# Kernel optimization log

Hardware: AMD Instinct MI355X
Metric: run time of the kernel (lower is better)

## Reference

```python
import jax, jax.numpy as jnp
import numpy as np

D_MODEL = 1024
N_HEADS = 16
D_K = D_MODEL // N_HEADS
D_FF = 4096
EPS = 1e-5


def _layernorm(x, g, b):
    mu = jnp.mean(x, axis=-1, keepdims=True)
    var = jnp.var(x, axis=-1, keepdims=True)
    return (x - mu) * jax.lax.rsqrt(var + EPS) * g + b


def setup_inputs() -> dict:
    key = jax.random.key(0)
    ks = jax.random.split(key, 12)
    s = 0.02
    x = jax.random.normal(ks[0], (2, 2048, D_MODEL), dtype=jnp.float32)
    # Linear weights stored [in, out] so y = x @ W + b
    wq = jax.random.normal(ks[1], (D_MODEL, D_MODEL), dtype=jnp.float32) * s
    wk = jax.random.normal(ks[2], (D_MODEL, D_MODEL), dtype=jnp.float32) * s
    wv = jax.random.normal(ks[3], (D_MODEL, D_MODEL), dtype=jnp.float32) * s
    wo = jax.random.normal(ks[4], (D_MODEL, D_MODEL), dtype=jnp.float32) * s
    bq = jnp.zeros((D_MODEL,), jnp.float32)
    bk = jnp.zeros((D_MODEL,), jnp.float32)
    bv = jnp.zeros((D_MODEL,), jnp.float32)
    bo = jnp.zeros((D_MODEL,), jnp.float32)
    ln1_g = jnp.ones((D_MODEL,), jnp.float32)
    ln1_b = jnp.zeros((D_MODEL,), jnp.float32)
    ln2_g = jnp.ones((D_MODEL,), jnp.float32)
    ln2_b = jnp.zeros((D_MODEL,), jnp.float32)
    w1 = jax.random.normal(ks[5], (D_MODEL, D_FF), dtype=jnp.float32) * s
    b1 = jnp.zeros((D_FF,), jnp.float32)
    w2 = jax.random.normal(ks[6], (D_FF, D_MODEL), dtype=jnp.float32) * s
    b2 = jnp.zeros((D_MODEL,), jnp.float32)
    return {"x": x, "wq": wq, "bq": bq, "wk": wk, "bk": bk, "wv": wv, "bv": bv,
            "wo": wo, "bo": bo, "ln1_g": ln1_g, "ln1_b": ln1_b,
            "ln2_g": ln2_g, "ln2_b": ln2_b, "w1": w1, "b1": b1, "w2": w2, "b2": b2}


def reference(x, wq, bq, wk, bk, wv, bv, wo, bo, ln1_g, ln1_b, ln2_g, ln2_b, w1, b1, w2, b2):
    B, S, _ = x.shape
    res = x
    # project and split heads: [B, S, H, Dk]
    q = (x @ wq + bq).reshape(B, S, N_HEADS, D_K)
    k = (x @ wk + bk).reshape(B, S, N_HEADS, D_K)
    v = (x @ wv + bv).reshape(B, S, N_HEADS, D_K)
    # full score matrix [B, H, Sq, Sk] (faithful to unfused original)
    scores = jnp.einsum('bqhd,bkhd->bhqk', q, k) / jnp.sqrt(jnp.float32(D_K))
    weights = jax.nn.softmax(scores, axis=-1)
    attn = jnp.einsum('bhqk,bkhd->bqhd', weights, v).reshape(B, S, D_MODEL)
    x = _layernorm(res + attn @ wo + bo, ln1_g, ln1_b)
    res = x
    h = jax.nn.relu(x @ w1 + b1)
    x = _layernorm(res + h @ w2 + b2, ln2_g, ln2_b)
    return x
```

## Files before the change

### kernel.cpp

```cpp
#include <hip/hip_runtime.h>
#include <hip/hip_bf16.h>
#include <stdint.h>


typedef __hip_bfloat16 bf16;
typedef short bf16x8 __attribute__((ext_vector_type(8)));
typedef float f32x4 __attribute__((ext_vector_type(4)));

#if __has_builtin(__builtin_amdgcn_exp2f)
#define EXP2F(x) __builtin_amdgcn_exp2f(x)
#else
#define EXP2F(x) exp2f(x)
#endif

__device__ __forceinline__ float bf2f_lo(unsigned u) { return __uint_as_float(u << 16); }
__device__ __forceinline__ float bf2f_hi(unsigned u) { return __uint_as_float(u & 0xffff0000u); }
__device__ __forceinline__ ushort f2bf(float f) {
  union { bf16 h; ushort u; } c; c.h = __float2bfloat16(f); return c.u;
}
__device__ __forceinline__ uint pk_bf16(float a, float b) {
  union { __hip_bfloat162 h2; uint u; } c;
  c.h2 = __float22bfloat162_rn(make_float2(a, b));
  return c.u;
}
__device__ __forceinline__ bool is_f32(const uint* probe) { return probe[0] == 0x3F800000u; }
__device__ __forceinline__ float ld_param(const void* p, size_t i, bool f32) {
  return f32 ? ((const float*)p)[i] : __bfloat162float(((const bf16*)p)[i]);
}

__device__ __forceinline__ void barrier_raw() {
  asm volatile("" ::: "memory");
  __builtin_amdgcn_s_barrier();
  asm volatile("" ::: "memory");
}
__device__ __forceinline__ void lgkm0() {
  asm volatile("s_waitcnt lgkmcnt(0)" ::: "memory");
}
__device__ __forceinline__ void glds16(const ushort* g, ushort* l) {
  __builtin_amdgcn_global_load_lds(
      (const __attribute__((address_space(1))) void*)g,
      (__attribute__((address_space(3))) void*)l, 16, 0, 0);
}

#define MFMA16(MH, NH)                                                        \
  do {                                                                        \
    _Pragma("unroll") for (int c_ = 0; c_ < 2; ++c_)                          \
    _Pragma("unroll") for (int fi_ = 0; fi_ < 4; ++fi_)                       \
    _Pragma("unroll") for (int gi_ = 0; gi_ < 2; ++gi_)                       \
      acc[(MH) * 4 + fi_][(NH) * 2 + gi_] =                                   \
          __builtin_amdgcn_mfma_f32_16x16x32_bf16(                            \
              areg[fi_][c_], breg[(NH) * 2 + gi_][c_],                        \
              acc[(MH) * 4 + fi_][(NH) * 2 + gi_], 0, 0, 0);                  \
  } while (0)

__device__ __forceinline__ void gemm256_body(
    const ushort* __restrict__ A, const ushort* __restrict__ BT,
    const void* __restrict__ bias, const void* __restrict__ res,
    void* __restrict__ C, int N_, int K_, int bm, int bn,
    int kb, int ke, int mode, const uint* probe) {
  __shared__ ushort As[2][16384];
  __shared__ ushort Bs[2][16384];

  const int tid = threadIdx.x;
  const int wave = tid >> 6;
  const int lane = tid & 63;
  const int wm = wave >> 2;
  const int wn = wave & 3;
  const int m16 = lane & 15;
  const int quad = lane >> 4;
  const int nt = (ke - kb) >> 6;

  const int srow = lane >> 2;
  const int skc = ((lane & 3) * 8) ^ (((lane >> 5) & 1) << 4);
  const ushort* pA = A + (size_t)(bm * 256 + wave * 16 + srow) * K_ + kb + skc;
  const ushort* pB = BT + (size_t)(bn * 256 + wave * 16 + srow) * K_ + kb + skc;
  const size_t hstep = (size_t)128 * K_;
  ushort* dA = &As[0][0] + wave * 1024;
  ushort* dB = &Bs[0][0] + wave * 1024;

  auto stageA = [&](int b, int half, int t) {
    const ushort* g = pA + (size_t)half * hstep + t * 64;
    ushort* d = dA + b * 16384 + half * 8192;
    glds16(g, d);
    glds16(g + 32, d + 512);
  };
  auto stageB = [&](int b, int half, int t) {
    const ushort* g = pB + (size_t)half * hstep + t * 64;
    ushort* d = dB + b * 16384 + half * 8192;
    glds16(g, d);
    glds16(g + 32, d + 512);
  };

  const int fr_off = m16 * 32 + ((quad * 8) ^ (((m16 >> 3) & 1) << 4));
  const ushort* rA = &As[0][0] + fr_off;
  const ushort* rB = &Bs[0][0] + fr_off;
  auto ldA = [&](int b, int f, int c) {
    return *(const bf16x8*)(rA + b * 16384 +
                            ((f >> 2) * 8 + wm * 4 + (f & 3)) * 1024 + c * 512);
  };
  auto ldB = [&](int b, int g, int c) {
    return *(const bf16x8*)(rB + b * 16384 +
                            ((g >> 1) * 8 + wn * 2 + (g & 1)) * 1024 + c * 512);
  };

  f32x4 acc[8][4];
#pragma unroll
  for (int f = 0; f < 8; ++f)
#pragma unroll
    for (int g = 0; g < 4; ++g) acc[f][g] = (f32x4){0.f, 0.f, 0.f, 0.f};
  bf16x8 areg[4][2], breg[4][2];

  stageA(0, 0, 0); stageB(0, 0, 0); stageA(0, 1, 0); stageB(0, 1, 0);
  if (nt > 1) { stageA(1, 0, 1); stageB(1, 0, 1); }
  asm volatile("s_waitcnt vmcnt(4)" ::: "memory");
  barrier_raw();

  for (int t = 0; t < nt; ++t) {
    const int b = t & 1, bo = b ^ 1;
#pragma unroll
    for (int fi = 0; fi < 4; ++fi) { areg[fi][0] = ldA(b, fi, 0); areg[fi][1] = ldA(b, fi, 1); }
#pragma unroll
    for (int gi = 0; gi < 2; ++gi) { breg[gi][0] = ldB(b, gi, 0); breg[gi][1] = ldB(b, gi, 1); }
    if (t + 1 < nt) stageA(bo, 1, t + 1);
    barrier_raw(); lgkm0();
    __builtin_amdgcn_s_setprio(1); MFMA16(0, 0); __builtin_amdgcn_s_setprio(0);
    barrier_raw();
#pragma unroll
    for (int gi = 2; gi < 4; ++gi) { breg[gi][0] = ldB(b, gi, 0); breg[gi][1] = ldB(b, gi, 1); }
    if (t + 1 < nt) stageB(bo, 1, t + 1);
    barrier_raw(); lgkm0();
    __builtin_amdgcn_s_setprio(1); MFMA16(0, 1); __builtin_amdgcn_s_setprio(0);
    barrier_raw();
#pragma unroll
    for (int fi = 0; fi < 4; ++fi) { areg[fi][0] = ldA(b, fi + 4, 0); areg[fi][1] = ldA(b, fi + 4, 1); }
    if (t + 2 < nt) stageA(b, 0, t + 2);
    barrier_raw(); lgkm0();
    __builtin_amdgcn_s_setprio(1); MFMA16(1, 0); __builtin_amdgcn_s_setprio(0);
    barrier_raw();
    if (t + 2 < nt) stageB(b, 0, t + 2);
    barrier_raw(); lgkm0();
    __builtin_amdgcn_s_setprio(1); MFMA16(1, 1); __builtin_amdgcn_s_setprio(0);
    if (t + 2 < nt) asm volatile("s_waitcnt vmcnt(4)" ::: "memory");
    else            asm volatile("s_waitcnt vmcnt(0)" ::: "memory");
    barrier_raw();
  }

  const bool F32 = is_f32(probe);
#pragma unroll
  for (int g = 0; g < 4; ++g) {
    const int col = bn * 256 + (g >> 1) * 128 + wn * 32 + (g & 1) * 16 + m16;
    const float bv = (mode >= 3) ? 0.f : ld_param(bias, col, F32);
#pragma unroll
    for (int f = 0; f < 8; ++f) {
      const int rowb = bm * 256 + (f >> 2) * 128 + wm * 64 + (f & 3) * 16 + quad * 4;
#pragma unroll
      for (int r = 0; r < 4; ++r) {
        const int row = rowb + r;
        float v = acc[f][g][r] + bv;
        if (mode == 1) v = fmaxf(v, 0.f);
        if (mode == 2) v += __bfloat162float(((const bf16*)res)[(size_t)row * N_ + col]);
        if (mode == 2 || mode == 3) ((float*)C)[(size_t)row * N_ + col] = v;
        else ((bf16*)C)[(size_t)row * N_ + col] = __float2bfloat16(v);
      }
    }
  }
}

__global__ __launch_bounds__(512, 2) void gemm256_qkv(
    const ushort* A, const ushort* BT0, const ushort* BT1, const ushort* BT2,
    const void* b0, const void* b1, const void* b2,
    bf16* C0, bf16* C1, bf16* C2, const uint* probe) {
  const int sel = blockIdx.y >> 2, bn = blockIdx.y & 3;
  const ushort* BT = sel == 0 ? BT0 : (sel == 1 ? BT1 : BT2);
  const void* bb = sel == 0 ? b0 : (sel == 1 ? b1 : b2);
  bf16* C = sel == 0 ? C0 : (sel == 1 ? C1 : C2);
  gemm256_body(A, BT, bb, nullptr, C, 1024, 1024, blockIdx.x, bn, 0, 1024, 0, probe);
}
__global__ __launch_bounds__(512, 2) void gemm256_ffn1(
    const ushort* A, const ushort* BT, const void* bias, bf16* C, const uint* probe) {
  gemm256_body(A, BT, bias, nullptr, C, 4096, 1024,
               blockIdx.x, blockIdx.y, 0, 1024, 1, probe);
}
__global__ __launch_bounds__(512, 2) void gemm256_ffn2_sk4(
    const ushort* A, const ushort* BT,
    bf16* P0, bf16* P1, bf16* P2, bf16* P3, const uint* probe) {
  const int kz = blockIdx.z;
  bf16* C = kz == 0 ? P0 : kz == 1 ? P1 : kz == 2 ? P2 : P3;
  gemm256_body(A, BT, nullptr, nullptr, C, 1024, 4096, blockIdx.x, blockIdx.y,
               kz * 1024, kz * 1024 + 1024, 4, probe);
}
__global__ __launch_bounds__(512, 2) void gemm256_wo_sk4(
    const ushort* A, const ushort* BT,
    bf16* P0, bf16* P1, bf16* P2, bf16* P3, const uint* probe) {
  const int kz = blockIdx.z;
  bf16* C = kz == 0 ? P0 : kz == 1 ? P1 : kz == 2 ? P2 : P3;
  gemm256_body(A, BT, nullptr, nullptr, C, 1024, 1024, blockIdx.x, blockIdx.y,
               kz * 256, kz * 256 + 256, 4, probe);
}

__global__ __launch_bounds__(256) void transpose_all(
    const void* W0, const void* W1, const void* W2, const void* W3,
    const void* W4, const void* W5, const void* X6,
    ushort* D0, ushort* D1, ushort* D2, ushort* D3, ushort* D4, ushort* D5,
    ushort* D6, const uint* probe) {
  const int z = blockIdx.z;
  if (z == 6) {
    const bool F32 = is_f32(probe);
    const size_t i =
        ((size_t)(blockIdx.y * 128 + blockIdx.x) * 256 + threadIdx.x) * 4;
    if (F32) {
      const float4 a = *(const float4*)((const float*)X6 + i);
      uint2 o; o.x = pk_bf16(a.x, a.y); o.y = pk_bf16(a.z, a.w);
      *(uint2*)(D6 + i) = o;
    } else {
      *(uint2*)(D6 + i) = *(const uint2*)((const ushort*)X6 + i);
    }
    return;
  }
  if (z < 4 && blockIdx.x >= 32) return;
  int n0, k0, K_, N_;
  const void* W;
  ushort* D;
  if (z < 4) {
    n0 = blockIdx.x * 32; k0 = blockIdx.y * 32; K_ = 1024; N_ = 1024;
    W = z == 0 ? W0 : z == 1 ? W1 : z == 2 ? W2 : W3;
    D = z == 0 ? D0 : z == 1 ? D1 : z == 2 ? D2 : D3;
  } else if (z == 4) {
    n0 = blockIdx.x * 32; k0 = blockIdx.y * 32; K_ = 1024; N_ = 4096; W = W4; D = D4;
  } else {
    n0 = blockIdx.y * 32; k0 = blockIdx.x * 32; K_ = 4096; N_ = 1024; W = W5; D = D5;
  }
  const bool F32 = is_f32(probe);
  __shared__ ushort tile[32][33];
  const int tx = threadIdx.x & 31, ty = threadIdx.x >> 5;
#pragma unroll
  for (int i = 0; i < 32; i += 8) {
    const size_t src = (size_t)(k0 + ty + i) * N_ + n0 + tx;
    tile[ty + i][tx] = F32 ? f2bf(((const float*)W)[src]) : ((const ushort*)W)[src];
  }
  __syncthreads();
#pragma unroll
  for (int i = 0; i < 32; i += 8)
    D[(size_t)(n0 + ty + i) * K_ + k0 + tx] = tile[tx][ty + i];
}

__global__ __launch_bounds__(256) void transpose_v(
    const ushort* __restrict__ Vb, ushort* __restrict__ VTp) {
  __shared__ ushort t64[64][66];
  const int tid = threadIdx.x;
  const int ktb = blockIdx.x;
  const int bh = blockIdx.y;
  const int bb = bh >> 4, h = bh & 15;
  const size_t hb = ((size_t)bb * 2048) * 1024 + (size_t)h * 64;
  const int r = tid >> 2, c4 = (tid & 3) * 16;
  const ushort* src = Vb + hb + (size_t)(ktb * 64 + r) * 1024 + c4;
  *(uint4*)&t64[r][c4] = *(const uint4*)src;
  *(uint4*)&t64[r][c4 + 8] = *(const uint4*)(src + 8);
  __syncthreads();
  ushort vals[16];
#pragma unroll
  for (int j = 0; j < 16; ++j) {
    const int jj = c4 + j;
    const int k = 16 * (jj & 3) + 4 * ((jj >> 3) & 3) + 2 * (jj >> 5) + ((jj & 7) >> 2);
    vals[j] = t64[k][r];
  }
  ushort* dst = VTp + (size_t)bh * 131072 + (size_t)r * 2048 + ktb * 64 + c4;
  *(uint4*)dst = *(uint4*)&vals[0];
  *(uint4*)(dst + 8) = *(uint4*)&vals[8];
}

template <bool OUT_EXT, bool RES_EXT>
__global__ __launch_bounds__(256) void ln4_kernel(
    const ushort* __restrict__ P0, const ushort* __restrict__ P1,
    const ushort* __restrict__ P2, const ushort* __restrict__ P3,
    const void* __restrict__ res, const void* __restrict__ bias,
    const void* __restrict__ g, const void* __restrict__ bta,
    void* __restrict__ out, const uint* probe) {
  const bool F32 = is_f32(probe);
  const int row = blockIdx.x;
  const int tid = threadIdx.x;
  const size_t base = (size_t)row * 1024 + tid * 4;
  float xv[4];
  if (RES_EXT && F32) {
    const float4 a = *(const float4*)((const float*)res + base);
    xv[0] = a.x; xv[1] = a.y; xv[2] = a.z; xv[3] = a.w;
  } else {
    const uint2 ur = *(const uint2*)((const ushort*)res + base);
    xv[0] = bf2f_lo(ur.x); xv[1] = bf2f_hi(ur.x);
    xv[2] = bf2f_lo(ur.y); xv[3] = bf2f_hi(ur.y);
  }
#pragma unroll
  for (int i = 0; i < 4; ++i) xv[i] += ld_param(bias, tid * 4 + i, F32);
  auto addv = [&](const ushort* P) {
    const uint2 u = *(const uint2*)(P + base);
    xv[0] += bf2f_lo(u.x); xv[1] += bf2f_hi(u.x);
    xv[2] += bf2f_lo(u.y); xv[3] += bf2f_hi(u.y);
  };
  addv(P0); addv(P1); addv(P2); addv(P3);
  float s = xv[0] + xv[1] + xv[2] + xv[3];
  float ss = xv[0] * xv[0] + xv[1] * xv[1] + xv[2] * xv[2] + xv[3] * xv[3];
#pragma unroll
  for (int o = 32; o > 0; o >>= 1) { s += __shfl_down(s, o); ss += __shfl_down(ss, o); }
  __shared__ float red[8];
  if ((tid & 63) == 0) { red[tid >> 6] = s; red[4 + (tid >> 6)] = ss; }
  __syncthreads();
  s = red[0] + red[1] + red[2] + red[3];
  ss = red[4] + red[5] + red[6] + red[7];
  const float mu = s * (1.f / 1024.f);
  const float rstd = rsqrtf(ss * (1.f / 1024.f) - mu * mu + 1e-5f);
#pragma unroll
  for (int i = 0; i < 4; ++i) {
    const size_t idx = base + i;
    const float y = (xv[i] - mu) * rstd * ld_param(g, tid * 4 + i, F32) +
                    ld_param(bta, tid * 4 + i, F32);
    if (OUT_EXT && F32) ((float*)out)[idx] = y;
    else ((bf16*)out)[idx] = __float2bfloat16(y);
  }
}

__global__ __launch_bounds__(256, 4) void attn_mfma(
    const ushort* __restrict__ Qm, const ushort* __restrict__ Km,
    const ushort* __restrict__ VTp, ushort* __restrict__ Om) {
  __shared__ ushort Ks[2][4096];
  __shared__ ushort Vs[2][4096];

  const int tid = threadIdx.x;
  const int wave = tid >> 6, lane = tid & 63;
  const int m16 = lane & 15, quad = lane >> 4;

  const int g = blockIdx.x;
  const int slot = g >> 3;
  const int bh = (g & 7) * 4 + (slot >> 5);
  const int qt = slot & 31;
  const int bb = bh >> 4, h = bh & 15;
  const size_t hb = ((size_t)bb * 2048) * 1024 + (size_t)h * 64;
  const size_t vo = (size_t)bh * 131072;
  const int q0 = qt * 64 + wave * 16;

  const float QS = 0.125f * 1.44269504f;
  const int swz = (m16 >> 3) << 4;
  const int rdo = m16 * 32 + ((quad * 8) ^ swz);

  bf16x8 qf[2];
#pragma unroll
  for (int c = 0; c < 2; ++c) {
    const uint4 u = *(const uint4*)(Qm + hb + (size_t)(q0 + m16) * 1024 + c * 32 + quad * 8);
    const uint w[4] = {u.x, u.y, u.z, u.w};
    bf16x8 f;
#pragma unroll
    for (int j = 0; j < 4; ++j) {
      const uint p = pk_bf16(bf2f_lo(w[j]) * QS, bf2f_hi(w[j]) * QS);
      f[2 * j]     = (short)(p & 0xffffu);
      f[2 * j + 1] = (short)(p >> 16);
    }
    qf[c] = f;
  }

  f32x4 zero = {0.f, 0.f, 0.f, 0.f};
  f32x4 acc[4];
#pragma unroll
  for (int jd = 0; jd < 4; ++jd) acc[jd] = zero;
  float lp = 0.f;

  const int srow = lane >> 2;
  const int skc = ((lane & 3) * 8) ^ ((lane >> 5) << 4);
  const ushort* pK = Km + hb + (size_t)(wave * 16 + srow) * 1024 + skc;
  const ushort* pV = VTp + vo + (size_t)(wave * 16 + srow) * 2048 + skc;
  ushort* dK = &Ks[0][0] + wave * 1024;
  ushort* dV = &Vs[0][0] + wave * 1024;

  glds16(pK, dK);
  glds16(pK + 32, dK + 512);
  glds16(pV, dV);
  glds16(pV + 32, dV + 512);
  asm volatile("s_waitcnt vmcnt(0)" ::: "memory");

  for (int kt = 0; kt < 2048; kt += 64) {
    const int b = (kt >> 6) & 1;
    __syncthreads();
    if (kt + 64 < 2048) {
      const ushort* gk = pK + (size_t)(kt + 64) * 1024;
      const ushort* gv = pV + (kt + 64);
      ushort* dk2 = dK + (b ^ 1) * 4096;
      ushort* dv2 = dV + (b ^ 1) * 4096;
      glds16(gk, dk2);
      glds16(gk + 32, dk2 + 512);
      glds16(gv, dv2);
      glds16(gv + 32, dv2 + 512);
    }

    f32x4 s[4];
#pragma unroll
    for (int jn = 0; jn < 4; ++jn) s[jn] = zero;
    __builtin_amdgcn_s_setprio(1);
#pragma unroll
    for (int c = 0; c < 2; ++c) {
      bf16x8 kb4[4];
#pragma unroll
      for (int jn = 0; jn < 4; ++jn)
        kb4[jn] = *(const bf16x8*)&Ks[b][jn * 1024 + c * 512 + rdo];
#pragma unroll
      for (int jn = 0; jn < 4; ++jn)
        s[jn] = __builtin_amdgcn_mfma_f32_16x16x32_bf16(kb4[jn], qf[c], s[jn], 0, 0, 0);
    }
    __builtin_amdgcn_s_setprio(0);

    float pr[4][4];
#pragma unroll
    for (int jn = 0; jn < 4; ++jn) {
#pragma unroll
      for (int r = 0; r < 4; ++r) pr[jn][r] = EXP2F(s[jn][r]);
      lp += (pr[jn][0] + pr[jn][1]) + (pr[jn][2] + pr[jn][3]);
    }
    bf16x8 paf[2];
#pragma unroll
    for (int c = 0; c < 2; ++c) {
      union { uint4 u4; bf16x8 v; } cvt;
      cvt.u4.x = pk_bf16(pr[0][2 * c], pr[1][2 * c]);
      cvt.u4.y = pk_bf16(pr[2][2 * c], pr[3][2 * c]);
      cvt.u4.z = pk_bf16(pr[0][2 * c + 1], pr[1][2 * c + 1]);
      cvt.u4.w = pk_bf16(pr[2][2 * c + 1], pr[3][2 * c + 1]);
      paf[c] = cvt.v;
    }

    __builtin_amdgcn_s_setprio(1);
#pragma unroll
    for (int c = 0; c < 2; ++c) {
      bf16x8 vb4[4];
#pragma unroll
      for (int jd = 0; jd < 4; ++jd)
        vb4[jd] = *(const bf16x8*)&Vs[b][jd * 1024 + c * 512 + rdo];
#pragma unroll
      for (int jd = 0; jd < 4; ++jd)
        acc[jd] = __builtin_amdgcn_mfma_f32_16x16x32_bf16(paf[c], vb4[jd], acc[jd], 0, 0, 0);
    }
    __builtin_amdgcn_s_setprio(0);
    asm volatile("s_waitcnt vmcnt(0)" ::: "memory");
  }

  float l = lp;
  l += __shfl_xor(l, 16);
  l += __shfl_xor(l, 32);
#pragma unroll
  for (int r = 0; r < 4; ++r) {
    const float inv = 1.f / __shfl(l, quad * 4 + r);
    const size_t rowoff = hb + (size_t)(q0 + quad * 4 + r) * 1024;
#pragma unroll
    for (int jd = 0; jd < 4; ++jd)
      Om[rowoff + jd * 16 + m16] = f2bf(acc[jd][r] * inv);
  }
}

extern "C" void kernel_launch(void* const* d_in, const int* in_sizes, int n_in,
                              void* d_out, int out_size, void* d_ws, size_t ws_size,
                              hipStream_t stream) {
  const void* x   = d_in[0];
  const void* wq  = d_in[1];
  const void* bq  = d_in[2];
  const void* wk  = d_in[3];
  const void* bk  = d_in[4];
  const void* wv  = d_in[5];
  const void* bv  = d_in[6];
  const void* wo  = d_in[7];
  const void* bo  = d_in[8];
  const uint* probe = (const uint*)d_in[9];
  const void* ln1g = d_in[9];
  const void* ln1b = d_in[10];
  const void* ln2g = d_in[11];
  const void* ln2b = d_in[12];
  const void* w1  = d_in[13];
  const void* b1  = d_in[14];
  const void* w2  = d_in[15];
  const void* b2  = d_in[16];

  char* ws = (char*)d_ws;
  const size_t MB = 1ull << 20;
  ushort* wqT = (ushort*)(ws + 0 * MB);
  ushort* wkT = (ushort*)(ws + 2 * MB);
  ushort* wvT = (ushort*)(ws + 4 * MB);
  ushort* woT = (ushort*)(ws + 6 * MB);
  ushort* w1T = (ushort*)(ws + 8 * MB);
  ushort* w2T = (ushort*)(ws + 16 * MB);
  ushort* Qb  = (ushort*)(ws + 24 * MB);
  ushort* Kb  = (ushort*)(ws + 32 * MB);
  ushort* Vb  = (ushort*)(ws + 40 * MB);
  ushort* VTp = (ushort*)(ws + 48 * MB);
  ushort* Xb  = (ushort*)(ws + 64 * MB);
  ushort* AO  = (ushort*)(ws + 72 * MB);
  ushort* W0  = (ushort*)(ws + 24 * MB);
  ushort* W1  = (ushort*)(ws + 32 * MB);
  ushort* W2  = (ushort*)(ws + 40 * MB);
  ushort* W3  = (ushort*)(ws + 48 * MB);
  ushort* X1  = (ushort*)(ws + 56 * MB);
  ushort* Hb  = (ushort*)(ws + 24 * MB);
  ushort* P2a = (ushort*)(ws + 0 * MB);
  ushort* P2b = (ushort*)(ws + 8 * MB);
  ushort* P2c = (ushort*)(ws + 64 * MB);
  ushort* P2d = (ushort*)(ws + 72 * MB);

  const dim3 blk(256);
  const dim3 blk512(512);
  transpose_all<<<dim3(128, 32, 7), blk, 0, stream>>>(
      wq, wk, wv, wo, w1, w2, x, wqT, wkT, wvT, woT, w1T, w2T, Xb, probe);

  gemm256_qkv<<<dim3(16, 12), blk512, 0, stream>>>(
      Xb, wqT, wkT, wvT, bq, bk, bv, (bf16*)Qb, (bf16*)Kb, (bf16*)Vb, probe);
  transpose_v<<<dim3(32, 32), blk, 0, stream>>>(Vb, VTp);
  attn_mfma<<<dim3(1024), blk, 0, stream>>>(Qb, Kb, VTp, AO);
  gemm256_wo_sk4<<<dim3(16, 4, 4), blk512, 0, stream>>>(
      AO, woT, (bf16*)W0, (bf16*)W1, (bf16*)W2, (bf16*)W3, probe);
  ln4_kernel<false, true><<<dim3(4096), blk, 0, stream>>>(
      W0, W1, W2, W3, x, bo, ln1g, ln1b, X1, probe);
  gemm256_ffn1<<<dim3(16, 16), blk512, 0, stream>>>(X1, w1T, b1, (bf16*)Hb, probe);
  gemm256_ffn2_sk4<<<dim3(16, 4, 4), blk512, 0, stream>>>(
      Hb, w2T, (bf16*)P2a, (bf16*)P2b, (bf16*)P2c, (bf16*)P2d, probe);
  ln4_kernel<true, false><<<dim3(4096), blk, 0, stream>>>(
      P2a, P2b, P2c, P2d, X1, b2, ln2g, ln2b, d_out, probe);
}
```

Before: 347.6 us.

## Triple-buffer K/V tiles in attention kernel with two-stage prefetch

The attention kernel moves from double to triple buffering of the K/V shared-memory tiles. It now prefetches two tiles ahead and waits with vmcnt(4) instead of draining all loads each iteration, so global-to-LDS latency is hidden over a longer window. This raises LDS use to 48KB per block and lowers the launch-bounds occupancy hint from 4 to 3 blocks, which may cost latency hiding across blocks.

```diff
diff --git a/kernel.cpp b/kernel.cpp
--- a/kernel.cpp
+++ b/kernel.cpp
@@ -318,11 +318,11 @@
   }
 }
 
-__global__ __launch_bounds__(256, 4) void attn_mfma(
+__global__ __launch_bounds__(256, 3) void attn_mfma(
     const ushort* __restrict__ Qm, const ushort* __restrict__ Km,
     const ushort* __restrict__ VTp, ushort* __restrict__ Om) {
-  __shared__ ushort Ks[2][4096];
-  __shared__ ushort Vs[2][4096];
+  __shared__ ushort Ks[3][4096];
+  __shared__ ushort Vs[3][4096];
 
   const int tid = threadIdx.x;
   const int wave = tid >> 6, lane = tid & 63;
@@ -369,25 +369,26 @@
   ushort* dK = &Ks[0][0] + wave * 1024;
   ushort* dV = &Vs[0][0] + wave * 1024;
 
-  glds16(pK, dK);
-  glds16(pK + 32, dK + 512);
-  glds16(pV, dV);
-  glds16(pV + 32, dV + 512);
-  asm volatile("s_waitcnt vmcnt(0)" ::: "memory");
-
+  auto stage = [&](int buf, int kt_) {
+    const ushort* gk = pK + (size_t)kt_ * 1024;
+    const ushort* gv = pV + kt_;
+    ushort* dk2 = dK + buf * 4096;
+    ushort* dv2 = dV + buf * 4096;
+    glds16(gk, dk2);
+    glds16(gk + 32, dk2 + 512);
+    glds16(gv, dv2);
+    glds16(gv + 32, dv2 + 512);
+  };
+
+  stage(0, 0);
+  stage(1, 64);
+  asm volatile("s_waitcnt vmcnt(4)" ::: "memory");
+  __syncthreads();
+
+  int b = 0;
   for (int kt = 0; kt < 2048; kt += 64) {
-    const int b = (kt >> 6) & 1;
-    __syncthreads();
-    if (kt + 64 < 2048) {
-      const ushort* gk = pK + (size_t)(kt + 64) * 1024;
-      const ushort* gv = pV + (kt + 64);
-      ushort* dk2 = dK + (b ^ 1) * 4096;
-      ushort* dv2 = dV + (b ^ 1) * 4096;
-      glds16(gk, dk2);
-      glds16(gk + 32, dk2 + 512);
-      glds16(gv, dv2);
-      glds16(gv + 32, dv2 + 512);
-    }
+    const int bs = b >= 1 ? b - 1 : 2;
+    if (kt + 128 < 2048) stage(bs, kt + 128);
 
     f32x4 s[4];
 #pragma unroll
@@ -398,7 +399,7 @@
       bf16x8 kb4[4];
 #pragma unroll
       for (int jn = 0; jn < 4; ++jn)
-        kb4[jn] = *(const bf16x8*)&Ks[b][jn * 1024 + c * 512 + rdo];
+        kb4[jn] = *(const bf16x8*)&Ks[0][b * 4096 + jn * 1024 + c * 512 + rdo];
 #pragma unroll
       for (int jn = 0; jn < 4; ++jn)
         s[jn] = __builtin_amdgcn_mfma_f32_16x16x32_bf16(kb4[jn], qf[c], s[jn], 0, 0, 0);
@@ -429,13 +430,17 @@
       bf16x8 vb4[4];
 #pragma unroll
       for (int jd = 0; jd < 4; ++jd)
-        vb4[jd] = *(const bf16x8*)&Vs[b][jd * 1024 + c * 512 + rdo];
+        vb4[jd] = *(const bf16x8*)&Vs[0][b * 4096 + jd * 1024 + c * 512 + rdo];
 #pragma unroll
       for (int jd = 0; jd < 4; ++jd)
         acc[jd] = __builtin_amdgcn_mfma_f32_16x16x32_bf16(paf[c], vb4[jd], acc[jd], 0, 0, 0);
     }
     __builtin_amdgcn_s_setprio(0);
-    asm volatile("s_waitcnt vmcnt(0)" ::: "memory");
+
+    if (kt + 128 < 2048) asm volatile("s_waitcnt vmcnt(4)" ::: "memory");
+    else                 asm volatile("s_waitcnt vmcnt(0)" ::: "memory");
+    __syncthreads();
+    b = b == 2 ? 0 : b + 1;
   }
 
   float l = lp;
```

New measurement: 364.3 us. 1.05x slower.
